# Kernel optimization log

Measured on AMD Instinct MI355X. Metric: run time of the kernel, lower is better.

The kernel has to match this reference:

```python
import jax, jax.numpy as jnp
import numpy as np

N_NODES = 50000
N_EDGES = 800000
D_HIDDEN = 128
N_LAYERS = 3


def setup_inputs() -> dict:
    key = jax.random.key(0)
    k1, k2, k3 = jax.random.split(key, 3)
    x = jax.random.normal(k1, (N_NODES, D_HIDDEN), dtype=jnp.float32)
    edge_index = jax.random.randint(k2, (2, N_EDGES), 0, N_NODES, dtype=jnp.int32)
    # per-layer GCNConv params: weight [d,d], bias [d] (PyG lin has bias merged into conv bias)
    Ws = jax.random.normal(k3, (N_LAYERS, D_HIDDEN, D_HIDDEN), dtype=jnp.float32) / np.sqrt(D_HIDDEN).astype(np.float32)
    bs = jnp.zeros((N_LAYERS, D_HIDDEN), dtype=jnp.float32)
    return {"x": x, "edge_index": edge_index, "Ws": Ws, "bs": bs}


def reference(x, edge_index, Ws, bs):
    n = x.shape[0]
    # PyG GCNConv default: add self-loops, symmetric degree normalization.
    loops = jnp.arange(n, dtype=edge_index.dtype)
    src = jnp.concatenate([edge_index[0], loops])  # message sources (x_j)
    dst = jnp.concatenate([edge_index[1], loops])  # aggregation targets
    deg = jax.ops.segment_sum(jnp.ones_like(src, dtype=x.dtype), dst, num_segments=n)
    dinv = jnp.where(deg > 0, jax.lax.rsqrt(deg), jnp.zeros_like(deg))
    norm = dinv[src] * dinv[dst]  # [E+N]; edge_index is static across layers so compute once
    for l in range(Ws.shape[0]):
        h = x @ Ws[l]                                  # dense linear [N, d]
        msg = h[src] * norm[:, None]                   # gather + normalize [E+N, d]
        x = jax.ops.segment_sum(msg, dst, num_segments=n) + bs[l]  # scatter-add
    # single GELU applied after the final layer (per the original forward)
    x = jax.nn.gelu(x, approximate=False)
    return x
```

## Files before the change

### kernel.cpp

```cpp
#include <hip/hip_runtime.h>
#include <math.h>

#define D 128

typedef __attribute__((ext_vector_type(8))) short short8v;
typedef __attribute__((ext_vector_type(4))) float f32x4;

__device__ __forceinline__ unsigned short f2bf(float x) {
    unsigned int u = __float_as_uint(x);
    unsigned int r = (u + 0x7FFFu + ((u >> 16) & 1u)) >> 16;
    return (unsigned short)r;
}
__device__ __forceinline__ float bf2f(unsigned short b) {
    return __uint_as_float(((unsigned int)b) << 16);
}


__global__ void zero_k(int* __restrict__ cnt, int n) {
    int i = blockIdx.x * blockDim.x + threadIdx.x;
    if (i < n) cnt[i] = 0;
}

__global__ void rank_k(const int* __restrict__ dst, int E,
                       int* __restrict__ cnt, unsigned short* __restrict__ rank) {
    int e = blockIdx.x * blockDim.x + threadIdx.x;
    if (e < E) rank[e] = (unsigned short)atomicAdd(&cnt[dst[e]], 1);
}

__global__ __launch_bounds__(1024) void scan_a(const int* __restrict__ cnt, int N,
                                               int* __restrict__ part, int* __restrict__ bsum) {
    __shared__ int s[1024];
    int i = blockIdx.x * 1024 + threadIdx.x;
    int v = (i < N) ? cnt[i] : 0;
    s[threadIdx.x] = v;
    __syncthreads();
    for (int off = 1; off < 1024; off <<= 1) {
        int add = (threadIdx.x >= off) ? s[threadIdx.x - off] : 0;
        __syncthreads();
        s[threadIdx.x] += add;
        __syncthreads();
    }
    if (i < N) part[i] = s[threadIdx.x] - v;
    if (threadIdx.x == 1023) bsum[blockIdx.x] = s[1023];
}

__global__ __launch_bounds__(256) void scan_c(const int* __restrict__ cnt, int* __restrict__ part,
                                              const int* __restrict__ bsum,
                                              float* __restrict__ dinv, int N, int E) {
    __shared__ int s_pref;
    int chunk = blockIdx.x >> 2;
    if (threadIdx.x < 64) {
        int v = (threadIdx.x < chunk) ? bsum[threadIdx.x] : 0;
#pragma unroll
        for (int off = 1; off < 64; off <<= 1) v += __shfl_xor(v, off);
        if (threadIdx.x == 0) s_pref = v;
    }
    __syncthreads();
    int i = blockIdx.x * blockDim.x + threadIdx.x;
    if (i < N) {
        part[i] = part[i] + s_pref;
        dinv[i] = rsqrtf((float)(cnt[i] + 1));
    }
    if (i == 0) part[N] = E;
}

__global__ void fill_k(const int* __restrict__ src, const int* __restrict__ dst,
                       const unsigned short* __restrict__ rank, const int* __restrict__ rp,
                       int E, unsigned short* __restrict__ ssrc) {
    int e = blockIdx.x * blockDim.x + threadIdx.x;
    if (e < E) {
        int p = rp[dst[e]] + (int)rank[e];
        ssrc[p] = (unsigned short)src[e];
    }
}


__global__ void wsplit_k(const float* __restrict__ Wp, short* __restrict__ BFh,
                         short* __restrict__ BFl, int total) {
    int idx = blockIdx.x * blockDim.x + threadIdx.x;
    if (idx >= total) return;
    int i    = idx & 7;
    int lane = (idx >> 3) & 63;
    int ct   = (idx >> 9) & 7;
    int ks   = (idx >> 12) & 3;
    int l    = idx >> 14;
    int k = ks * 32 + (lane >> 4) * 8 + i;
    int n = ct * 16 + (lane & 15);
    float w = Wp[(size_t)l * (D * D) + (size_t)k * D + n];
    unsigned short h = f2bf(w);
    float lo = w - bf2f(h);
    BFh[idx] = (short)h;
    BFl[idx] = (short)f2bf(lo);
}


__global__ __launch_bounds__(256) void gemm_k(const float* __restrict__ X,
                                              const short* __restrict__ BFh,
                                              const short* __restrict__ BFl,
                                              const float* __restrict__ dinv,
                                              unsigned short* __restrict__ Hb, int M) {
    int lane = threadIdx.x & 63;
    int wv = threadIdx.x >> 6;
    int rowBase = blockIdx.x * 64 + wv * 16;
    int arow = rowBase + (lane & 15);
    bool aval = arow < M;
    const float* xr = X + (size_t)arow * D + (lane >> 4) * 8;

    short8v ah[4], al[4];
#pragma unroll
    for (int ks = 0; ks < 4; ++ks) {
        float4 p = make_float4(0.f, 0.f, 0.f, 0.f);
        float4 q = make_float4(0.f, 0.f, 0.f, 0.f);
        if (aval) {
            p = *(const float4*)(xr + ks * 32);
            q = *(const float4*)(xr + ks * 32 + 4);
        }
        float v[8] = {p.x, p.y, p.z, p.w, q.x, q.y, q.z, q.w};
#pragma unroll
        for (int i = 0; i < 8; ++i) {
            unsigned short h = f2bf(v[i]);
            ah[ks][i] = (short)h;
            al[ks][i] = (short)f2bf(v[i] - bf2f(h));
        }
    }

    int rb = rowBase + (lane >> 4) * 4;
    float dsc[4];
#pragma unroll
    for (int i = 0; i < 4; ++i) dsc[i] = (rb + i < M) ? dinv[rb + i] : 0.f;

    const short8v* Bh = (const short8v*)BFh;
    const short8v* Bl = (const short8v*)BFl;
#pragma unroll
    for (int ct = 0; ct < 8; ++ct) {
        short8v bh[4], bl[4];
#pragma unroll
        for (int ks = 0; ks < 4; ++ks) {
            bh[ks] = Bh[(ks * 8 + ct) * 64 + lane];
            bl[ks] = Bl[(ks * 8 + ct) * 64 + lane];
        }
        f32x4 acc = {0.f, 0.f, 0.f, 0.f};
#pragma unroll
        for (int ks = 0; ks < 4; ++ks) {
            acc = __builtin_amdgcn_mfma_f32_16x16x32_bf16(ah[ks], bh[ks], acc, 0, 0, 0);
            acc = __builtin_amdgcn_mfma_f32_16x16x32_bf16(al[ks], bh[ks], acc, 0, 0, 0);
            acc = __builtin_amdgcn_mfma_f32_16x16x32_bf16(ah[ks], bl[ks], acc, 0, 0, 0);
        }
        int c = ct * 16 + (lane & 15);
#pragma unroll
        for (int i = 0; i < 4; ++i) {
            int r = rb + i;
            if (r < M) Hb[(size_t)r * D + c] = f2bf(dsc[i] * acc[i]);
        }
    }
}


__device__ __forceinline__ float gelu_f(float x) {
    return 0.5f * x * (1.0f + erff(x * 0.70710678118654752f));
}

__global__ __launch_bounds__(256) void agg_k(const unsigned short* __restrict__ Hb,
                                             const int* __restrict__ rp,
                                             const unsigned short* __restrict__ ssrc,
                                             const float* __restrict__ dinv,
                                             const float* __restrict__ bias,
                                             float* __restrict__ out, int N, int doGelu) {
    int node = blockIdx.x * 4 + (threadIdx.x >> 6);
    int lane = threadIdx.x & 63;
    if (node >= N) return;
    const uint4* __restrict__ hb4 = (const uint4*)Hb;
    int grp = lane >> 4;
    int sub = lane & 15;

    float acc[8];
#pragma unroll
    for (int i = 0; i < 8; ++i) acc[i] = 0.f;

    int e0 = rp[node];
    int e1 = rp[node + 1];
    for (int base = e0; base < e1; base += 64) {
        int idxv = 0;
        if (base + lane < e1) idxv = (int)ssrc[base + lane];
        int cnt = e1 - base; if (cnt > 64) cnt = 64;
        for (int c = 0; c < cnt; c += 16) {
            uint4 v[4];
#pragma unroll
            for (int j = 0; j < 4; ++j) {
                int row = __shfl(idxv, c + 4 * j + grp);
                v[j] = hb4[(size_t)row * 16 + sub];
            }
#pragma unroll
            for (int j = 0; j < 4; ++j) {
                bool ok = (base + c + 4 * j + grp) < e1;
                unsigned int w;
                w = ok ? v[j].x : 0u;
                acc[0] += __uint_as_float(w << 16); acc[1] += __uint_as_float(w & 0xFFFF0000u);
                w = ok ? v[j].y : 0u;
                acc[2] += __uint_as_float(w << 16); acc[3] += __uint_as_float(w & 0xFFFF0000u);
                w = ok ? v[j].z : 0u;
                acc[4] += __uint_as_float(w << 16); acc[5] += __uint_as_float(w & 0xFFFF0000u);
                w = ok ? v[j].w : 0u;
                acc[6] += __uint_as_float(w << 16); acc[7] += __uint_as_float(w & 0xFFFF0000u);
            }
        }
    }
#pragma unroll
    for (int i = 0; i < 8; ++i) {
        acc[i] += __shfl_xor(acc[i], 16);
        acc[i] += __shfl_xor(acc[i], 32);
    }
    if (lane < 16) {
        uint4 sv = hb4[(size_t)node * 16 + lane];
        acc[0] += __uint_as_float(sv.x << 16); acc[1] += __uint_as_float(sv.x & 0xFFFF0000u);
        acc[2] += __uint_as_float(sv.y << 16); acc[3] += __uint_as_float(sv.y & 0xFFFF0000u);
        acc[4] += __uint_as_float(sv.z << 16); acc[5] += __uint_as_float(sv.z & 0xFFFF0000u);
        acc[6] += __uint_as_float(sv.w << 16); acc[7] += __uint_as_float(sv.w & 0xFFFF0000u);
        float dn = dinv[node];
        float4 b0 = ((const float4*)bias)[lane * 2];
        float4 b1 = ((const float4*)bias)[lane * 2 + 1];
        float r[8];
        r[0] = dn * acc[0] + b0.x; r[1] = dn * acc[1] + b0.y;
        r[2] = dn * acc[2] + b0.z; r[3] = dn * acc[3] + b0.w;
        r[4] = dn * acc[4] + b1.x; r[5] = dn * acc[5] + b1.y;
        r[6] = dn * acc[6] + b1.z; r[7] = dn * acc[7] + b1.w;
        if (doGelu) {
#pragma unroll
            for (int i = 0; i < 8; ++i) r[i] = gelu_f(r[i]);
        }
        float4 o0 = make_float4(r[0], r[1], r[2], r[3]);
        float4 o1 = make_float4(r[4], r[5], r[6], r[7]);
        ((float4*)out)[(size_t)node * 32 + lane * 2]     = o0;
        ((float4*)out)[(size_t)node * 32 + lane * 2 + 1] = o1;
    }
}


extern "C" void kernel_launch(void* const* d_in, const int* in_sizes, int n_in,
                              void* d_out, int out_size, void* d_ws, size_t ws_size,
                              hipStream_t stream) {
    const float* X  = (const float*)d_in[0];
    const int*   EI = (const int*)d_in[1];
    const float* Wp = (const float*)d_in[2];
    const float* bp = (const float*)d_in[3];
    float* OUT = (float*)d_out;

    int N = in_sizes[0] / D;
    int E = in_sizes[1] / 2;
    int L = in_sizes[3] / D;
    const int* src = EI;
    const int* dst = EI + E;

    char* w = (char*)d_ws;
    auto alloc = [&](size_t bytes) {
        char* p = w;
        w += (bytes + 255) & ~(size_t)255;
        return p;
    };
    unsigned short* HB = (unsigned short*)alloc((size_t)N * D * sizeof(unsigned short));
    float* XB   = (float*)alloc((size_t)N * D * sizeof(float));
    float* DINV = (float*)alloc((size_t)N * sizeof(float));
    int*   RP   = (int*)alloc((size_t)(N + 1) * sizeof(int));
    int*   CNT  = (int*)alloc((size_t)N * sizeof(int));
    int*   BSUM = (int*)alloc(4096 * sizeof(int));
    unsigned short* RANK = (unsigned short*)alloc((size_t)E * sizeof(unsigned short));
    unsigned short* SSRC = (unsigned short*)alloc(((size_t)E + 64) * sizeof(unsigned short));
    short* BFH  = (short*)alloc((size_t)L * D * D * sizeof(short));
    short* BFL  = (short*)alloc((size_t)L * D * D * sizeof(short));
    (void)ws_size; (void)n_in; (void)out_size;

    zero_k<<<(N + 255) / 256, 256, 0, stream>>>(CNT, N);

    int eb = (E + 255) / 256;
    rank_k<<<eb, 256, 0, stream>>>(dst, E, CNT, RANK);
    int nb = (N + 1023) / 1024;
    scan_a<<<nb, 1024, 0, stream>>>(CNT, N, RP, BSUM);
    scan_c<<<(N + 255) / 256, 256, 0, stream>>>(CNT, RP, BSUM, DINV, N, E);
    fill_k<<<eb, 256, 0, stream>>>(src, dst, RANK, RP, E, SSRC);

    int wtot = L * D * D;
    wsplit_k<<<(wtot + 255) / 256, 256, 0, stream>>>(Wp, BFH, BFL, wtot);

    int gb = (N + 63) / 64;
    int ab = (N + 3) / 4;
    for (int l = 0; l < L; ++l) {
        const float* xin = (l == 0) ? X : XB;
        gemm_k<<<gb, 256, 0, stream>>>(xin, BFH + (size_t)l * D * D, BFL + (size_t)l * D * D,
                                       DINV, HB, N);
        float* o = (l == L - 1) ? OUT : XB;
        agg_k<<<ab, 256, 0, stream>>>(HB, RP, SSRC, DINV, bp + (size_t)l * D, o, N,
                                      (l == L - 1) ? 1 : 0);
    }
}
```

Before: 210.8 us.

## Fuse aggregation of layer l with GEMM of layer l+1 into one kernel

Adds an aggmm_k kernel that gathers and normalizes neighbor features for 64 nodes per block, splits the result into bf16 hi/lo in shared memory, and immediately multiplies by the next layer's weights with MFMA. This removes the fp32 intermediate X write and read between layers and cuts two kernel launches. The tradeoff is a different work mapping: each wave now walks 16 nodes serially with one 32-bit load per lane (the old agg_k used 16-byte loads), and the block count is smaller, so latency hiding in the gather may drop. The layer count is hardcoded to 3 in the host launch sequence.

Result: slower. 218.8 us (+3.8%).

```diff
diff --git a/kernel.cpp b/kernel.cpp
--- a/kernel.cpp
+++ b/kernel.cpp
@@ -156,6 +156,107 @@
 }
 
 
+__global__ __launch_bounds__(256) void aggmm_k(const unsigned short* __restrict__ Hin,
+                                               const int* __restrict__ rp,
+                                               const unsigned short* __restrict__ ssrc,
+                                               const float* __restrict__ dinv,
+                                               const float* __restrict__ bias,
+                                               const short* __restrict__ BFh,
+                                               const short* __restrict__ BFl,
+                                               unsigned short* __restrict__ Hout, int N) {
+    __shared__ unsigned int AH[4][16][68];
+    __shared__ unsigned int AL[4][16][68];
+    int lane = threadIdx.x & 63;
+    int wv = threadIdx.x >> 6;
+    int rowBase = blockIdx.x * 64 + wv * 16;
+    const unsigned int* __restrict__ hb = (const unsigned int*)Hin;
+    float2 bv = ((const float2*)bias)[lane];
+
+    for (int rr = 0; rr < 16; ++rr) {
+        int node = rowBase + rr;
+        float r0 = 0.f, r1 = 0.f;
+        if (node < N) {
+            unsigned int sv = hb[(size_t)node * 64 + lane];
+            float ax = __uint_as_float(sv << 16);
+            float ay = __uint_as_float(sv & 0xFFFF0000u);
+            float bx = 0.f, by = 0.f;
+            int e0 = rp[node];
+            int e1 = rp[node + 1];
+            for (int base = e0; base < e1; base += 64) {
+                int idxv = 0;
+                if (base + lane < e1) idxv = (int)ssrc[base + lane];
+                int cnt = e1 - base; if (cnt > 64) cnt = 64;
+                for (int c = 0; c < cnt; c += 16) {
+                    int s[16];
+                    unsigned int v[16];
+#pragma unroll
+                    for (int j = 0; j < 16; ++j) s[j] = __shfl(idxv, c + j);
+#pragma unroll
+                    for (int j = 0; j < 16; ++j) v[j] = hb[(size_t)s[j] * 64 + lane];
+#pragma unroll
+                    for (int j = 0; j < 16; ++j) {
+                        unsigned int m = (c + j < cnt) ? v[j] : 0u;
+                        float fx = __uint_as_float(m << 16);
+                        float fy = __uint_as_float(m & 0xFFFF0000u);
+                        if (j & 1) { bx += fx; by += fy; }
+                        else       { ax += fx; ay += fy; }
+                    }
+                }
+            }
+            ax += bx; ay += by;
+            float dn = dinv[node];
+            r0 = dn * ax + bv.x;
+            r1 = dn * ay + bv.y;
+        }
+        unsigned short h0 = f2bf(r0);
+        unsigned short h1 = f2bf(r1);
+        unsigned short l0 = f2bf(r0 - bf2f(h0));
+        unsigned short l1 = f2bf(r1 - bf2f(h1));
+        AH[wv][rr][lane] = (unsigned int)h0 | ((unsigned int)h1 << 16);
+        AL[wv][rr][lane] = (unsigned int)l0 | ((unsigned int)l1 << 16);
+    }
+
+    short8v ah[4], al[4];
+    int arow = lane & 15;
+    int kq = (lane >> 4) * 4;
+#pragma unroll
+    for (int ks = 0; ks < 4; ++ks) {
+        ah[ks] = *(const short8v*)&AH[wv][arow][ks * 16 + kq];
+        al[ks] = *(const short8v*)&AL[wv][arow][ks * 16 + kq];
+    }
+
+    int rb = rowBase + (lane >> 4) * 4;
+    float dsc[4];
+#pragma unroll
+    for (int i = 0; i < 4; ++i) dsc[i] = (rb + i < N) ? dinv[rb + i] : 0.f;
+
+    const short8v* Bh = (const short8v*)BFh;
+    const short8v* Bl = (const short8v*)BFl;
+#pragma unroll
+    for (int ct = 0; ct < 8; ++ct) {
+        short8v bh[4], bl[4];
+#pragma unroll
+        for (int ks = 0; ks < 4; ++ks) {
+            bh[ks] = Bh[(ks * 8 + ct) * 64 + lane];
+            bl[ks] = Bl[(ks * 8 + ct) * 64 + lane];
+        }
+        f32x4 acc = {0.f, 0.f, 0.f, 0.f};
+#pragma unroll
+        for (int ks = 0; ks < 4; ++ks) {
+            acc = __builtin_amdgcn_mfma_f32_16x16x32_bf16(ah[ks], bh[ks], acc, 0, 0, 0);
+            acc = __builtin_amdgcn_mfma_f32_16x16x32_bf16(al[ks], bh[ks], acc, 0, 0, 0);
+            acc = __builtin_amdgcn_mfma_f32_16x16x32_bf16(ah[ks], bl[ks], acc, 0, 0, 0);
+        }
+        int c = ct * 16 + (lane & 15);
+#pragma unroll
+        for (int i = 0; i < 4; ++i) {
+            int r = rb + i;
+            if (r < N) Hout[(size_t)r * D + c] = f2bf(dsc[i] * acc[i]);
+        }
+    }
+}
+
+
 __device__ __forceinline__ float gelu_f(float x) {
     return 0.5f * x * (1.0f + erff(x * 0.70710678118654752f));
 }
@@ -165,7 +266,7 @@
                                              const unsigned short* __restrict__ ssrc,
                                              const float* __restrict__ dinv,
                                              const float* __restrict__ bias,
-                                             float* __restrict__ out, int N, int doGelu) {
+                                             float* __restrict__ out, int N) {
     int node = blockIdx.x * 4 + (threadIdx.x >> 6);
     int lane = threadIdx.x & 63;
     if (node >= N) return;
@@ -224,10 +325,8 @@
         r[2] = dn * acc[2] + b0.z; r[3] = dn * acc[3] + b0.w;
         r[4] = dn * acc[4] + b1.x; r[5] = dn * acc[5] + b1.y;
         r[6] = dn * acc[6] + b1.z; r[7] = dn * acc[7] + b1.w;
-        if (doGelu) {
-#pragma unroll
-            for (int i = 0; i < 8; ++i) r[i] = gelu_f(r[i]);
-        }
+#pragma unroll
+        for (int i = 0; i < 8; ++i) r[i] = gelu_f(r[i]);
         float4 o0 = make_float4(r[0], r[1], r[2], r[3]);
         float4 o1 = make_float4(r[4], r[5], r[6], r[7]);
         ((float4*)out)[(size_t)node * 32 + lane * 2]     = o0;
@@ -257,8 +356,8 @@
         w += (bytes + 255) & ~(size_t)255;
         return p;
     };
-    unsigned short* HB = (unsigned short*)alloc((size_t)N * D * sizeof(unsigned short));
-    float* XB   = (float*)alloc((size_t)N * D * sizeof(float));
+    unsigned short* HA = (unsigned short*)alloc((size_t)N * D * sizeof(unsigned short));
+    unsigned short* HBuf = (unsigned short*)alloc((size_t)N * D * sizeof(unsigned short));
     float* DINV = (float*)alloc((size_t)N * sizeof(float));
     int*   RP   = (int*)alloc((size_t)(N + 1) * sizeof(int));
     int*   CNT  = (int*)alloc((size_t)N * sizeof(int));
@@ -282,13 +381,13 @@
     wsplit_k<<<(wtot + 255) / 256, 256, 0, stream>>>(Wp, BFH, BFL, wtot);
 
     int gb = (N + 63) / 64;
+    gemm_k<<<gb, 256, 0, stream>>>(X, BFH, BFL, DINV, HA, N);
+    aggmm_k<<<gb, 256, 0, stream>>>(HA, RP, SSRC, DINV, bp,
+                                    BFH + (size_t)1 * D * D, BFL + (size_t)1 * D * D,
+                                    HBuf, N);
+    aggmm_k<<<gb, 256, 0, stream>>>(HBuf, RP, SSRC, DINV, bp + D,
+                                    BFH + (size_t)2 * D * D, BFL + (size_t)2 * D * D,
+                                    HA, N);
     int ab = (N + 3) / 4;
-    for (int l = 0; l < L; ++l) {
-        const float* xin = (l == 0) ? X : XB;
-        gemm_k<<<gb, 256, 0, stream>>>(xin, BFH + (size_t)l * D * D, BFL + (size_t)l * D * D,
-                                       DINV, HB, N);
-        float* o = (l == L - 1) ? OUT : XB;
-        agg_k<<<ab, 256, 0, stream>>>(HB, RP, SSRC, DINV, bp + (size_t)l * D, o, N,
-                                      (l == L - 1) ? 1 : 0);
-    }
-}
+    agg_k<<<ab, 256, 0, stream>>>(HA, RP, SSRC, DINV, bp + 2 * D, OUT, N);
+}
```

## Fuse prep kernels, overlap CSR fill with first GEMM, store intermediates as bf16 hi/lo

Applied to the files above, without the earlier changes.

Merges the weight split and the count zeroing into one prep kernel. The CSR fill now runs as extra blocks of the first GEMM launch, which removes two launches and lets the scatter overlap with MFMA work. Intermediate layer outputs are written as bf16 high/low pairs rather than fp32, so the next GEMM loads them directly without converting. Traffic per intermediate is unchanged (4 bytes per element), but the conversion moves from the GEMM into the aggregation epilogue, and the layer loop is unrolled to hardcode three layers.

Result: faster. 206.4 us (-2.1%).

```diff
diff --git a/kernel.cpp b/kernel.cpp
--- a/kernel.cpp
+++ b/kernel.cpp
@@ -16,10 +16,26 @@
 }
 
 
-__global__ void zero_k(int* __restrict__ cnt, int n) {
-    int i = blockIdx.x * blockDim.x + threadIdx.x;
-    if (i < n) cnt[i] = 0;
-}
+__global__ void prep_k(const float* __restrict__ Wp, short* __restrict__ BFh,
+                       short* __restrict__ BFl, int wtot,
+                       int* __restrict__ cnt, int N) {
+    int idx = blockIdx.x * blockDim.x + threadIdx.x;
+    if (idx < wtot) {
+        int i    = idx & 7;
+        int lane = (idx >> 3) & 63;
+        int ct   = (idx >> 9) & 7;
+        int ks   = (idx >> 12) & 3;
+        int l    = idx >> 14;
+        int k = ks * 32 + (lane >> 4) * 8 + i;
+        int n = ct * 16 + (lane & 15);
+        float w = Wp[(size_t)l * (D * D) + (size_t)k * D + n];
+        unsigned short h = f2bf(w);
+        BFh[idx] = (short)h;
+        BFl[idx] = (short)f2bf(w - bf2f(h));
+    }
+    if (idx < N) cnt[idx] = 0;
+}
+
 
 __global__ void rank_k(const int* __restrict__ dst, int E,
                        int* __restrict__ cnt, unsigned short* __restrict__ rank) {
@@ -64,44 +80,52 @@
     if (i == 0) part[N] = E;
 }
 
-__global__ void fill_k(const int* __restrict__ src, const int* __restrict__ dst,
-                       const unsigned short* __restrict__ rank, const int* __restrict__ rp,
-                       int E, unsigned short* __restrict__ ssrc) {
-    int e = blockIdx.x * blockDim.x + threadIdx.x;
-    if (e < E) {
-        int p = rp[dst[e]] + (int)rank[e];
-        ssrc[p] = (unsigned short)src[e];
-    }
-}
-
-
-__global__ void wsplit_k(const float* __restrict__ Wp, short* __restrict__ BFh,
-                         short* __restrict__ BFl, int total) {
-    int idx = blockIdx.x * blockDim.x + threadIdx.x;
-    if (idx >= total) return;
-    int i    = idx & 7;
-    int lane = (idx >> 3) & 63;
-    int ct   = (idx >> 9) & 7;
-    int ks   = (idx >> 12) & 3;
-    int l    = idx >> 14;
-    int k = ks * 32 + (lane >> 4) * 8 + i;
-    int n = ct * 16 + (lane & 15);
-    float w = Wp[(size_t)l * (D * D) + (size_t)k * D + n];
-    unsigned short h = f2bf(w);
-    float lo = w - bf2f(h);
-    BFh[idx] = (short)h;
-    BFl[idx] = (short)f2bf(lo);
-}
-
-
-__global__ __launch_bounds__(256) void gemm_k(const float* __restrict__ X,
-                                              const short* __restrict__ BFh,
-                                              const short* __restrict__ BFl,
-                                              const float* __restrict__ dinv,
-                                              unsigned short* __restrict__ Hb, int M) {
-    int lane = threadIdx.x & 63;
-    int wv = threadIdx.x >> 6;
-    int rowBase = blockIdx.x * 64 + wv * 16;
+
+__device__ __forceinline__ void mfma_phase(short8v ah[4], short8v al[4],
+                                           const short* __restrict__ BFh,
+                                           const short* __restrict__ BFl,
+                                           const float* __restrict__ dinv,
+                                           unsigned short* __restrict__ Hb, int M,
+                                           int rowBase, int lane) {
+    int rb = rowBase + (lane >> 4) * 4;
+    float dsc[4];
+#pragma unroll
+    for (int i = 0; i < 4; ++i) dsc[i] = (rb + i < M) ? dinv[rb + i] : 0.f;
+
+    const short8v* Bh = (const short8v*)BFh;
+    const short8v* Bl = (const short8v*)BFl;
+#pragma unroll
+    for (int ct = 0; ct < 8; ++ct) {
+        short8v bh[4], bl[4];
+#pragma unroll
+        for (int ks = 0; ks < 4; ++ks) {
+            bh[ks] = Bh[(ks * 8 + ct) * 64 + lane];
+            bl[ks] = Bl[(ks * 8 + ct) * 64 + lane];
+        }
+        f32x4 acc = {0.f, 0.f, 0.f, 0.f};
+#pragma unroll
+        for (int ks = 0; ks < 4; ++ks) {
+            acc = __builtin_amdgcn_mfma_f32_16x16x32_bf16(ah[ks], bh[ks], acc, 0, 0, 0);
+            acc = __builtin_amdgcn_mfma_f32_16x16x32_bf16(al[ks], bh[ks], acc, 0, 0, 0);
+            acc = __builtin_amdgcn_mfma_f32_16x16x32_bf16(ah[ks], bl[ks], acc, 0, 0, 0);
+        }
+        int c = ct * 16 + (lane & 15);
+#pragma unroll
+        for (int i = 0; i < 4; ++i) {
+            int r = rb + i;
+            if (r < M) Hb[(size_t)r * D + c] = f2bf(dsc[i] * acc[i]);
+        }
+    }
+}
+
+__device__ __forceinline__ void gemm_body(const float* __restrict__ X,
+                                          const short* __restrict__ BFh,
+                                          const short* __restrict__ BFl,
+                                          const float* __restrict__ dinv,
+                                          unsigned short* __restrict__ Hb, int M,
+                                          int bid, int tid) {
+    int lane = tid & 63;
+    int rowBase = bid * 64 + (tid >> 6) * 16;
     int arow = rowBase + (lane & 15);
     bool aval = arow < M;
     const float* xr = X + (size_t)arow * D + (lane >> 4) * 8;
@@ -123,34 +147,54 @@
             al[ks][i] = (short)f2bf(v[i] - bf2f(h));
         }
     }
-
-    int rb = rowBase + (lane >> 4) * 4;
-    float dsc[4];
-#pragma unroll
-    for (int i = 0; i < 4; ++i) dsc[i] = (rb + i < M) ? dinv[rb + i] : 0.f;
-
-    const short8v* Bh = (const short8v*)BFh;
-    const short8v* Bl = (const short8v*)BFl;
-#pragma unroll
-    for (int ct = 0; ct < 8; ++ct) {
-        short8v bh[4], bl[4];
-#pragma unroll
-        for (int ks = 0; ks < 4; ++ks) {
-            bh[ks] = Bh[(ks * 8 + ct) * 64 + lane];
-            bl[ks] = Bl[(ks * 8 + ct) * 64 + lane];
-        }
-        f32x4 acc = {0.f, 0.f, 0.f, 0.f};
-#pragma unroll
-        for (int ks = 0; ks < 4; ++ks) {
-            acc = __builtin_amdgcn_mfma_f32_16x16x32_bf16(ah[ks], bh[ks], acc, 0, 0, 0);
-            acc = __builtin_amdgcn_mfma_f32_16x16x32_bf16(al[ks], bh[ks], acc, 0, 0, 0);
-            acc = __builtin_amdgcn_mfma_f32_16x16x32_bf16(ah[ks], bl[ks], acc, 0, 0, 0);
-        }
-        int c = ct * 16 + (lane & 15);
-#pragma unroll
-        for (int i = 0; i < 4; ++i) {
-            int r = rb + i;
-            if (r < M) Hb[(size_t)r * D + c] = f2bf(dsc[i] * acc[i]);
+    mfma_phase(ah, al, BFh, BFl, dinv, Hb, M, rowBase, lane);
+}
+
+__global__ __launch_bounds__(256) void gemm2_k(const unsigned short* __restrict__ XH,
+                                               const unsigned short* __restrict__ XL,
+                                               const short* __restrict__ BFh,
+                                               const short* __restrict__ BFl,
+                                               const float* __restrict__ dinv,
+                                               unsigned short* __restrict__ Hb, int M) {
+    int lane = threadIdx.x & 63;
+    int rowBase = blockIdx.x * 64 + (threadIdx.x >> 6) * 16;
+    int arow = rowBase + (lane & 15);
+    bool aval = arow < M;
+    const unsigned short* xh = XH + (size_t)arow * D + (lane >> 4) * 8;
+    const unsigned short* xl = XL + (size_t)arow * D + (lane >> 4) * 8;
+
+    short8v ah[4], al[4];
+#pragma unroll
+    for (int ks = 0; ks < 4; ++ks) {
+        short8v zh = {0,0,0,0,0,0,0,0};
+        short8v zl = {0,0,0,0,0,0,0,0};
+        if (aval) {
+            zh = *(const short8v*)(xh + ks * 32);
+            zl = *(const short8v*)(xl + ks * 32);
+        }
+        ah[ks] = zh;
+        al[ks] = zl;
+    }
+    mfma_phase(ah, al, BFh, BFl, dinv, Hb, M, rowBase, lane);
+}
+
+__global__ __launch_bounds__(256) void fillgemm_k(const float* __restrict__ X,
+                                                  const short* __restrict__ BFh,
+                                                  const short* __restrict__ BFl,
+                                                  const float* __restrict__ dinv,
+                                                  unsigned short* __restrict__ Hb, int M, int gb,
+                                                  const int* __restrict__ src,
+                                                  const int* __restrict__ dst,
+                                                  const unsigned short* __restrict__ rank,
+                                                  const int* __restrict__ rp, int E,
+                                                  unsigned short* __restrict__ ssrc) {
+    if ((int)blockIdx.x < gb) {
+        gemm_body(X, BFh, BFl, dinv, Hb, M, blockIdx.x, threadIdx.x);
+    } else {
+        int e = (blockIdx.x - gb) * blockDim.x + threadIdx.x;
+        if (e < E) {
+            int p = rp[dst[e]] + (int)rank[e];
+            ssrc[p] = (unsigned short)src[e];
         }
     }
 }
@@ -165,7 +209,10 @@
                                              const unsigned short* __restrict__ ssrc,
                                              const float* __restrict__ dinv,
                                              const float* __restrict__ bias,
-                                             float* __restrict__ out, int N, int doGelu) {
+                                             float* __restrict__ outF,
+                                             unsigned short* __restrict__ outH,
+                                             unsigned short* __restrict__ outL,
+                                             int N, int mode) {
     int node = blockIdx.x * 4 + (threadIdx.x >> 6);
     int lane = threadIdx.x & 63;
     if (node >= N) return;
@@ -224,14 +271,32 @@
         r[2] = dn * acc[2] + b0.z; r[3] = dn * acc[3] + b0.w;
         r[4] = dn * acc[4] + b1.x; r[5] = dn * acc[5] + b1.y;
         r[6] = dn * acc[6] + b1.z; r[7] = dn * acc[7] + b1.w;
-        if (doGelu) {
+        if (mode) {
 #pragma unroll
             for (int i = 0; i < 8; ++i) r[i] = gelu_f(r[i]);
-        }
-        float4 o0 = make_float4(r[0], r[1], r[2], r[3]);
-        float4 o1 = make_float4(r[4], r[5], r[6], r[7]);
-        ((float4*)out)[(size_t)node * 32 + lane * 2]     = o0;
-        ((float4*)out)[(size_t)node * 32 + lane * 2 + 1] = o1;
+            float4 o0 = make_float4(r[0], r[1], r[2], r[3]);
+            float4 o1 = make_float4(r[4], r[5], r[6], r[7]);
+            ((float4*)outF)[(size_t)node * 32 + lane * 2]     = o0;
+            ((float4*)outF)[(size_t)node * 32 + lane * 2 + 1] = o1;
+        } else {
+            unsigned short h[8], lo[8];
+#pragma unroll
+            for (int i = 0; i < 8; ++i) {
+                h[i]  = f2bf(r[i]);
+                lo[i] = f2bf(r[i] - bf2f(h[i]));
+            }
+            uint4 ph, pl;
+            ph.x = (unsigned int)h[0]  | ((unsigned int)h[1] << 16);
+            ph.y = (unsigned int)h[2]  | ((unsigned int)h[3] << 16);
+            ph.z = (unsigned int)h[4]  | ((unsigned int)h[5] << 16);
+            ph.w = (unsigned int)h[6]  | ((unsigned int)h[7] << 16);
+            pl.x = (unsigned int)lo[0] | ((unsigned int)lo[1] << 16);
+            pl.y = (unsigned int)lo[2] | ((unsigned int)lo[3] << 16);
+            pl.z = (unsigned int)lo[4] | ((unsigned int)lo[5] << 16);
+            pl.w = (unsigned int)lo[6] | ((unsigned int)lo[7] << 16);
+            ((uint4*)outH)[(size_t)node * 16 + lane] = ph;
+            ((uint4*)outL)[(size_t)node * 16 + lane] = pl;
+        }
     }
 }
 
@@ -257,8 +322,9 @@
         w += (bytes + 255) & ~(size_t)255;
         return p;
     };
-    unsigned short* HB = (unsigned short*)alloc((size_t)N * D * sizeof(unsigned short));
-    float* XB   = (float*)alloc((size_t)N * D * sizeof(float));
+    unsigned short* HB  = (unsigned short*)alloc((size_t)(N + 64) * D * sizeof(unsigned short));
+    unsigned short* XH  = (unsigned short*)alloc((size_t)(N + 64) * D * sizeof(unsigned short));
+    unsigned short* XL  = (unsigned short*)alloc((size_t)(N + 64) * D * sizeof(unsigned short));
     float* DINV = (float*)alloc((size_t)N * sizeof(float));
     int*   RP   = (int*)alloc((size_t)(N + 1) * sizeof(int));
     int*   CNT  = (int*)alloc((size_t)N * sizeof(int));
@@ -269,26 +335,26 @@
     short* BFL  = (short*)alloc((size_t)L * D * D * sizeof(short));
     (void)ws_size; (void)n_in; (void)out_size;
 
-    zero_k<<<(N + 255) / 256, 256, 0, stream>>>(CNT, N);
+    int wtot = L * D * D;
+    int pb = ((N > wtot ? N : wtot) + 255) / 256;
+    prep_k<<<pb, 256, 0, stream>>>(Wp, BFH, BFL, wtot, CNT, N);
 
     int eb = (E + 255) / 256;
     rank_k<<<eb, 256, 0, stream>>>(dst, E, CNT, RANK);
     int nb = (N + 1023) / 1024;
     scan_a<<<nb, 1024, 0, stream>>>(CNT, N, RP, BSUM);
     scan_c<<<(N + 255) / 256, 256, 0, stream>>>(CNT, RP, BSUM, DINV, N, E);
-    fill_k<<<eb, 256, 0, stream>>>(src, dst, RANK, RP, E, SSRC);
-
-    int wtot = L * D * D;
-    wsplit_k<<<(wtot + 255) / 256, 256, 0, stream>>>(Wp, BFH, BFL, wtot);
 
     int gb = (N + 63) / 64;
+    fillgemm_k<<<gb + eb, 256, 0, stream>>>(X, BFH, BFL, DINV, HB, N, gb,
+                                            src, dst, RANK, RP, E, SSRC);
+
     int ab = (N + 3) / 4;
-    for (int l = 0; l < L; ++l) {
-        const float* xin = (l == 0) ? X : XB;
-        gemm_k<<<gb, 256, 0, stream>>>(xin, BFH + (size_t)l * D * D, BFL + (size_t)l * D * D,
-                                       DINV, HB, N);
-        float* o = (l == L - 1) ? OUT : XB;
-        agg_k<<<ab, 256, 0, stream>>>(HB, RP, SSRC, DINV, bp + (size_t)l * D, o, N,
-                                      (l == L - 1) ? 1 : 0);
-    }
-}
+    agg_k<<<ab, 256, 0, stream>>>(HB, RP, SSRC, DINV, bp, nullptr, XH, XL, N, 0);
+    gemm2_k<<<gb, 256, 0, stream>>>(XH, XL, BFH + (size_t)1 * D * D, BFL + (size_t)1 * D * D,
+                                    DINV, HB, N);
+    agg_k<<<ab, 256, 0, stream>>>(HB, RP, SSRC, DINV, bp + D, nullptr, XH, XL, N, 0);
+    gemm2_k<<<gb, 256, 0, stream>>>(XH, XL, BFH + (size_t)2 * D * D, BFL + (size_t)2 * D * D,
+                                    DINV, HB, N);
+    agg_k<<<ab, 256, 0, stream>>>(HB, RP, SSRC, DINV, bp + 2 * D, OUT, nullptr, nullptr, N, 1);
+}
```
